# Kernel tuning notes

Hardware: AMD Instinct MI355X
Metric: run time of the kernel (lower is better)

The kernel has to match this reference:

```python
import jax, jax.numpy as jnp
import numpy as np

PROJ = 8192     # projDim
THRESH = 1e-8   # numerical-stability epsilon for signed sqrt
L2_EPS = 1e-12  # eps of torch F.normalize


def setup_inputs() -> dict:
    key = jax.random.key(0)
    k1, k2, k3, k4, k5 = jax.random.split(key, 5)
    B, C, H, W = 16, 512, 14, 14
    x = jax.random.normal(k1, (B, C, H, W), dtype=jnp.float32)
    h1 = jax.random.randint(k2, (C,), 0, PROJ, dtype=jnp.int32)
    h2 = jax.random.randint(k3, (C,), 0, PROJ, dtype=jnp.int32)
    s1 = (2 * jax.random.randint(k4, (C,), 0, 2) - 1).astype(jnp.float32)
    s2 = (2 * jax.random.randint(k5, (C,), 0, 2) - 1).astype(jnp.float32)
    return {"x": x, "s1": s1, "s2": s2, "h1": h1, "h2": h2}


def reference(x, s1, s2, h1, h2):
    # x: [B, C, H, W]; h*: [C] hash buckets in [0, PROJ); s*: [C] signs (+-1)
    B, C, H, W = x.shape
    x_flat = jnp.transpose(x, (0, 2, 3, 1)).reshape(-1, C)  # [N, C], N = B*H*W

    def count_sketch(s, h):
        # Equivalent to x_flat @ M with M[c, h[c]] = s[c]: scatter-add of
        # sign-weighted channels into PROJ bins.  -> [N, PROJ]
        return jax.ops.segment_sum((x_flat * s).T, h, num_segments=PROJ).T

    fft1 = jnp.fft.fft(count_sketch(s1, h1), axis=-1)
    fft2 = jnp.fft.fft(count_sketch(s2, h2), axis=-1)
    conv = jnp.fft.ifft(fft1 * fft2, axis=-1).real       # [N, PROJ]
    y = conv.reshape(B, H, W, PROJ).sum(axis=(1, 2))      # sum pool -> [B, PROJ]
    y = jnp.sign(y) * jnp.sqrt(jnp.abs(y) + THRESH)       # signed sqrt
    norm = jnp.linalg.norm(y, axis=1, keepdims=True)
    return y / jnp.maximum(norm, L2_EPS)                  # l2 normalize (dim=1)
```

## Files before the change

kernel.cpp:

```cpp
#include <hip/hip_runtime.h>
#include <math.h>

#define PROJ 8192
#define NB   16
#define NC   512
#define HW   196
#define KP   224
#define NROW (NB * NC)
#define XELE ((size_t)NROW * KP)

typedef __attribute__((ext_vector_type(8))) short bf16x8;
typedef __attribute__((ext_vector_type(4))) short short4v;
typedef __attribute__((ext_vector_type(4))) float f32x4;

__device__ __forceinline__ unsigned bf16_rne(float f) {
    unsigned u = __builtin_bit_cast(unsigned, f);
    return (u + 0x7fffu + ((u >> 16) & 1u)) >> 16;
}

__global__ __launch_bounds__(256)
void cbp_prep(const float* __restrict__ x,
              short* __restrict__ xh, short* __restrict__ xl) {
    const int id  = blockIdx.x * 256 + threadIdx.x;
    const int q   = id % 56;
    const int row = id / 56;
    float4 v = {0.f, 0.f, 0.f, 0.f};
    if (q < 49) v = *(const float4*)&x[(size_t)row * HW + 4 * q];
    const float f[4] = {v.x, v.y, v.z, v.w};
    short4v h, l;
#pragma unroll
    for (int c = 0; c < 4; ++c) {
        const unsigned hb = bf16_rne(f[c]);
        h[c] = (short)hb;
        l[c] = (short)bf16_rne(f[c] - __builtin_bit_cast(float, hb << 16));
    }
    *(short4v*)&xh[(size_t)row * KP + 4 * q] = h;
    *(short4v*)&xl[(size_t)row * KP + 4 * q] = l;
}

#define LOADFRAGS(buf, kc)                                             \
    {                                                                  \
        _Pragma("unroll")                                              \
        for (int i = 0; i < 2; ++i) {                                  \
            ah[buf][i] = *(const bf16x8*)&pAh[i * 3584 + (kc) * 32];   \
            al[buf][i] = *(const bf16x8*)&pAl[i * 3584 + (kc) * 32];   \
            bh[buf][i] = *(const bf16x8*)&pBh[i * 3584 + (kc) * 32];   \
            bl[buf][i] = *(const bf16x8*)&pBl[i * 3584 + (kc) * 32];   \
        }                                                              \
    }

__global__ __launch_bounds__(256, 4)
void cbp_gram(const short* __restrict__ xh, const short* __restrict__ xl,
              const float* __restrict__ s1, const float* __restrict__ s2,
              const int*   __restrict__ h1, const int*   __restrict__ h2,
              float* __restrict__ partials) {
    __shared__ float sk[PROJ];
    __shared__ int   rh1[64], rh2[64], ch1[64], ch2[64];
    __shared__ float rs1[64], rs2[64], cs1[64], cs2[64];

    const int tid = threadIdx.x;
    const int blk = blockIdx.x;
    const int xcd = blk & 7;
    const int idx = blk >> 3;
    const int hi  = (idx >= 36) ? 1 : 0;
    const int b   = 2 * xcd + hi;
    int I = 0, uu = idx - 36 * hi;
    while (uu >= 8 - I) { uu -= 8 - I; ++I; }
    const int J = I + uu;
    const int c1base = I * 64, c2base = J * 64;

    for (int i = tid; i < PROJ; i += 256) sk[i] = 0.f;
    if (tid < 64) {
        rh1[tid] = h1[c1base + tid]; rh2[tid] = h2[c1base + tid];
        rs1[tid] = s1[c1base + tid]; rs2[tid] = s2[c1base + tid];
    } else if (tid < 128) {
        const int t = tid - 64;
        ch1[t] = h1[c2base + t]; ch2[t] = h2[c2base + t];
        cs1[t] = s1[c2base + t]; cs2[t] = s2[c2base + t];
    }
    __syncthreads();

    const int lane = tid & 63, wave = tid >> 6;
    const int quad = lane >> 4, l15 = lane & 15;
    const int wr = (wave >> 1) * 32, wc = (wave & 1) * 32;

    const size_t rowA = ((size_t)b * NC + c1base + wr + l15) * KP + quad * 8;
    const size_t rowB = ((size_t)b * NC + c2base + wc + l15) * KP + quad * 8;
    const short* pAh = xh + rowA;  const short* pAl = xl + rowA;
    const short* pBh = xh + rowB;  const short* pBl = xl + rowB;

    f32x4 acc[2][2];
#pragma unroll
    for (int i = 0; i < 2; ++i)
#pragma unroll
        for (int j = 0; j < 2; ++j) acc[i][j] = (f32x4){0.f, 0.f, 0.f, 0.f};

    bf16x8 ah[2][2], al[2][2], bh[2][2], bl[2][2];
    LOADFRAGS(0, 0)
#pragma unroll
    for (int kc = 0; kc < 7; ++kc) {
        const int cur = kc & 1;
        if (kc < 6) LOADFRAGS(cur ^ 1, kc + 1)
#pragma unroll
        for (int i = 0; i < 2; ++i)
#pragma unroll
            for (int j = 0; j < 2; ++j) {
                acc[i][j] = __builtin_amdgcn_mfma_f32_16x16x32_bf16(ah[cur][i], bh[cur][j], acc[i][j], 0, 0, 0);
                acc[i][j] = __builtin_amdgcn_mfma_f32_16x16x32_bf16(ah[cur][i], bl[cur][j], acc[i][j], 0, 0, 0);
                acc[i][j] = __builtin_amdgcn_mfma_f32_16x16x32_bf16(al[cur][i], bh[cur][j], acc[i][j], 0, 0, 0);
            }
    }

    const bool offd = (I != J);
#pragma unroll
    for (int i = 0; i < 2; ++i) {
        const int r0 = wr + i * 16 + quad * 4;
#pragma unroll
        for (int j = 0; j < 2; ++j) {
            const int c = wc + j * 16 + l15;
            const int ch2v = ch2[c], ch1v = ch1[c];
            const float cs2v = cs2[c], cs1v = cs1[c];
#pragma unroll
            for (int rg = 0; rg < 4; ++rg) {
                const int r = r0 + rg;
                const float g = acc[i][j][rg];
                atomicAdd(&sk[(rh1[r] + ch2v) & (PROJ - 1)], rs1[r] * cs2v * g);
                if (offd)
                    atomicAdd(&sk[(ch1v + rh2[r]) & (PROJ - 1)], cs1v * rs2[r] * g);
            }
        }
    }
    __syncthreads();

    float4* dst = (float4*)(partials + (size_t)blk * PROJ);
    const float4* src = (const float4*)sk;
    for (int i = tid; i < PROJ / 4; i += 256) dst[i] = src[i];
}

__global__ __launch_bounds__(256)
void cbp_reduce(const float* __restrict__ partials, float* __restrict__ y,
                float* __restrict__ ssqp) {
    const int blk = blockIdx.x;
    const int xcd = blk & 7;
    const int k   = blk >> 3;
    const int hi  = k >> 5;
    const int seg = k & 31;
    const int b   = 2 * xcd + hi;
    const int tid = threadIdx.x;
    const int bin = seg * 256 + tid;

    float s = 0.f;
#pragma unroll
    for (int u = 0; u < 36; ++u) {
        int u2 = u + seg; if (u2 >= 36) u2 -= 36;
        const int pb = ((hi * 36 + u2) << 3) | xcd;
        s += partials[(size_t)pb * PROJ + bin];
    }

    const float m = sqrtf(fabsf(s) + 1e-8f);
    const float o = (s > 0.f) ? m : (s < 0.f ? -m : 0.f);
    y[b * PROJ + bin] = o;

    __shared__ float red[256];
    red[tid] = o * o;
    __syncthreads();
#pragma unroll
    for (int st = 128; st >= 1; st >>= 1) {
        if (tid < st) red[tid] += red[tid + st];
        __syncthreads();
    }
    if (tid == 0) ssqp[blk] = red[0];
}

__global__ __launch_bounds__(256)
void cbp_normalize(float* __restrict__ y, const float* __restrict__ ssqp) {
    const int b   = blockIdx.x >> 1;
    const int off = (blockIdx.x & 1) * 4096;
    const int tid = threadIdx.x;
    float ssq = 0.f;
#pragma unroll
    for (int seg = 0; seg < 32; ++seg)
        ssq += ssqp[(((b & 1) * 32 + seg) << 3) | (b >> 1)];
    const float inv = 1.0f / fmaxf(sqrtf(ssq), 1e-12f);

    float4* row = (float4*)&y[(size_t)b * PROJ + off];
#pragma unroll
    for (int j = 0; j < 4; ++j) {
        float4 v = row[j * 256 + tid];
        v.x *= inv; v.y *= inv; v.z *= inv; v.w *= inv;
        row[j * 256 + tid] = v;
    }
}

extern "C" void kernel_launch(void* const* d_in, const int* in_sizes, int n_in,
                              void* d_out, int out_size, void* d_ws, size_t ws_size,
                              hipStream_t stream) {
    const float* x  = (const float*)d_in[0];
    const float* s1 = (const float*)d_in[1];
    const float* s2 = (const float*)d_in[2];
    const int*   h1 = (const int*)d_in[3];
    const int*   h2 = (const int*)d_in[4];
    float* y = (float*)d_out;

    short* xh = (short*)d_ws;
    short* xl = xh + XELE;
    float* partials = (float*)(xl + XELE);
    float* ssqp = partials + (size_t)576 * PROJ;

    hipLaunchKernelGGL(cbp_prep, dim3(1792), dim3(256), 0, stream, x, xh, xl);
    hipLaunchKernelGGL(cbp_gram, dim3(576), dim3(256), 0, stream,
                       xh, xl, s1, s2, h1, h2, partials);
    hipLaunchKernelGGL(cbp_reduce, dim3(512), dim3(256), 0, stream,
                       partials, y, ssqp);
    hipLaunchKernelGGL(cbp_normalize, dim3(32), dim3(256), 0, stream, y, ssqp);
}
```

Before: 120.1 us.

## Compute full Gram tiles per block with 1024 threads, cutting partial sketches

```diff
diff --git a/kernel.cpp b/kernel.cpp
--- a/kernel.cpp
+++ b/kernel.cpp
@@ -6,8 +6,7 @@
 #define NC   512
 #define HW   196
 #define KP   224
-#define NROW (NB * NC)
-#define XELE ((size_t)NROW * KP)
+#define XELE ((size_t)NB * NC * KP)
 
 typedef __attribute__((ext_vector_type(8))) short bf16x8;
 typedef __attribute__((ext_vector_type(4))) short short4v;
@@ -38,54 +37,48 @@
     *(short4v*)&xl[(size_t)row * KP + 4 * q] = l;
 }
 
-#define LOADFRAGS(buf, kc)                                             \
-    {                                                                  \
-        _Pragma("unroll")                                              \
-        for (int i = 0; i < 2; ++i) {                                  \
-            ah[buf][i] = *(const bf16x8*)&pAh[i * 3584 + (kc) * 32];   \
-            al[buf][i] = *(const bf16x8*)&pAl[i * 3584 + (kc) * 32];   \
-            bh[buf][i] = *(const bf16x8*)&pBh[i * 3584 + (kc) * 32];   \
-            bl[buf][i] = *(const bf16x8*)&pBl[i * 3584 + (kc) * 32];   \
-        }                                                              \
-    }
-
-__global__ __launch_bounds__(256, 4)
+#define LOADFRAGS(buf, kc)                                          \
+    {                                                               \
+        const int off_ = (kc) * 32;                                 \
+        ah[buf][0] = *(const bf16x8*)&pAh[off_];                    \
+        ah[buf][1] = *(const bf16x8*)&pAh[16 * KP + off_];          \
+        al[buf][0] = *(const bf16x8*)&pAl[off_];                    \
+        al[buf][1] = *(const bf16x8*)&pAl[16 * KP + off_];          \
+        bh[buf][0] = *(const bf16x8*)&pBh[off_];                    \
+        bh[buf][1] = *(const bf16x8*)&pBh[16 * KP + off_];          \
+        bl[buf][0] = *(const bf16x8*)&pBl[off_];                    \
+        bl[buf][1] = *(const bf16x8*)&pBl[16 * KP + off_];          \
+    }
+
+__global__ __launch_bounds__(1024)
 void cbp_gram(const short* __restrict__ xh, const short* __restrict__ xl,
               const float* __restrict__ s1, const float* __restrict__ s2,
               const int*   __restrict__ h1, const int*   __restrict__ h2,
               float* __restrict__ partials) {
     __shared__ float sk[PROJ];
-    __shared__ int   rh1[64], rh2[64], ch1[64], ch2[64];
-    __shared__ float rs1[64], rs2[64], cs1[64], cs2[64];
 
     const int tid = threadIdx.x;
     const int blk = blockIdx.x;
     const int xcd = blk & 7;
-    const int idx = blk >> 3;
-    const int hi  = (idx >= 36) ? 1 : 0;
+    const int sub = blk >> 3;
+    const int hi  = sub >> 4;
+    const int q   = sub & 15;
     const int b   = 2 * xcd + hi;
-    int I = 0, uu = idx - 36 * hi;
-    while (uu >= 8 - I) { uu -= 8 - I; ++I; }
-    const int J = I + uu;
-    const int c1base = I * 64, c2base = J * 64;
-
-    for (int i = tid; i < PROJ; i += 256) sk[i] = 0.f;
-    if (tid < 64) {
-        rh1[tid] = h1[c1base + tid]; rh2[tid] = h2[c1base + tid];
-        rs1[tid] = s1[c1base + tid]; rs2[tid] = s2[c1base + tid];
-    } else if (tid < 128) {
-        const int t = tid - 64;
-        ch1[t] = h1[c2base + t]; ch2[t] = h2[c2base + t];
-        cs1[t] = s1[c2base + t]; cs2[t] = s2[c2base + t];
-    }
+
+    for (int i = tid; i < PROJ; i += 1024) sk[i] = 0.f;
     __syncthreads();
 
-    const int lane = tid & 63, wave = tid >> 6;
+    const int wave = tid >> 6, lane = tid & 63;
     const int quad = lane >> 4, l15 = lane & 15;
-    const int wr = (wave >> 1) * 32, wc = (wave & 1) * 32;
-
-    const size_t rowA = ((size_t)b * NC + c1base + wr + l15) * KP + quad * 8;
-    const size_t rowB = ((size_t)b * NC + c2base + wc + l15) * KP + quad * 8;
+    const int tile = q * 4 + (wave >> 2);
+    const int I = tile >> 3, J = tile & 7;
+    const int qr = ((wave >> 1) & 1) * 32;
+    const int qc = (wave & 1) * 32;
+    const int c1 = I * 64 + qr;
+    const int c2 = J * 64 + qc;
+
+    const size_t rowA = ((size_t)b * NC + c1 + l15) * KP + quad * 8;
+    const size_t rowB = ((size_t)b * NC + c2 + l15) * KP + quad * 8;
     const short* pAh = xh + rowA;  const short* pAl = xl + rowA;
     const short* pBh = xh + rowB;  const short* pBl = xl + rowB;
 
@@ -111,30 +104,37 @@
             }
     }
 
-    const bool offd = (I != J);
+    int   ha[2][4], hb[2];
+    float sa[2][4], sb[2];
 #pragma unroll
     for (int i = 0; i < 2; ++i) {
-        const int r0 = wr + i * 16 + quad * 4;
-#pragma unroll
-        for (int j = 0; j < 2; ++j) {
-            const int c = wc + j * 16 + l15;
-            const int ch2v = ch2[c], ch1v = ch1[c];
-            const float cs2v = cs2[c], cs1v = cs1[c];
+        const int r0 = c1 + i * 16 + quad * 4;
+#pragma unroll
+        for (int rg = 0; rg < 4; ++rg) {
+            ha[i][rg] = h1[r0 + rg];
+            sa[i][rg] = s1[r0 + rg];
+        }
+    }
+#pragma unroll
+    for (int j = 0; j < 2; ++j) {
+        const int c = c2 + j * 16 + l15;
+        hb[j] = h2[c];
+        sb[j] = s2[c];
+    }
+#pragma unroll
+    for (int i = 0; i < 2; ++i)
+#pragma unroll
+        for (int j = 0; j < 2; ++j)
 #pragma unroll
             for (int rg = 0; rg < 4; ++rg) {
-                const int r = r0 + rg;
-                const float g = acc[i][j][rg];
-                atomicAdd(&sk[(rh1[r] + ch2v) & (PROJ - 1)], rs1[r] * cs2v * g);
-                if (offd)
-                    atomicAdd(&sk[(ch1v + rh2[r]) & (PROJ - 1)], cs1v * rs2[r] * g);
+                const int bin = (ha[i][rg] + hb[j]) & (PROJ - 1);
+                atomicAdd(&sk[bin], sa[i][rg] * sb[j] * acc[i][j][rg]);
             }
-        }
-    }
     __syncthreads();
 
     float4* dst = (float4*)(partials + (size_t)blk * PROJ);
     const float4* src = (const float4*)sk;
-    for (int i = tid; i < PROJ / 4; i += 256) dst[i] = src[i];
+    for (int i = tid; i < PROJ / 4; i += 1024) dst[i] = src[i];
 }
 
 __global__ __launch_bounds__(256)
@@ -151,9 +151,9 @@
 
     float s = 0.f;
 #pragma unroll
-    for (int u = 0; u < 36; ++u) {
-        int u2 = u + seg; if (u2 >= 36) u2 -= 36;
-        const int pb = ((hi * 36 + u2) << 3) | xcd;
+    for (int u = 0; u < 16; ++u) {
+        const int u2 = (u + seg) & 15;
+        const int pb = ((hi * 16 + u2) << 3) | xcd;
         s += partials[(size_t)pb * PROJ + bin];
     }
 
@@ -205,10 +205,10 @@
     short* xh = (short*)d_ws;
     short* xl = xh + XELE;
     float* partials = (float*)(xl + XELE);
-    float* ssqp = partials + (size_t)576 * PROJ;
+    float* ssqp = partials + (size_t)256 * PROJ;
 
     hipLaunchKernelGGL(cbp_prep, dim3(1792), dim3(256), 0, stream, x, xh, xl);
-    hipLaunchKernelGGL(cbp_gram, dim3(576), dim3(256), 0, stream,
+    hipLaunchKernelGGL(cbp_gram, dim3(256), dim3(1024), 0, stream,
                        xh, xl, s1, s2, h1, h2, partials);
     hipLaunchKernelGGL(cbp_reduce, dim3(512), dim3(256), 0, stream,
                        partials, y, ssqp);
```

New measurement: 108.2 us. -9.9%, faster.

## Stage Gram operand tiles through LDS with coalesced loads and two-phase K split

Applied to the files above, without the earlier changes.

```diff
diff --git a/kernel.cpp b/kernel.cpp
--- a/kernel.cpp
+++ b/kernel.cpp
@@ -6,8 +6,8 @@
 #define NC   512
 #define HW   196
 #define KP   224
-#define NROW (NB * NC)
-#define XELE ((size_t)NROW * KP)
+#define LSK  132
+#define XELE ((size_t)NB * NC * KP)
 
 typedef __attribute__((ext_vector_type(8))) short bf16x8;
 typedef __attribute__((ext_vector_type(4))) short short4v;
@@ -21,9 +21,12 @@
 __global__ __launch_bounds__(256)
 void cbp_prep(const float* __restrict__ x,
               short* __restrict__ xh, short* __restrict__ xl) {
-    const int id  = blockIdx.x * 256 + threadIdx.x;
-    const int q   = id % 56;
-    const int row = id / 56;
+    const int e    = blockIdx.x & 7;
+    const int t    = blockIdx.x >> 3;
+    const int task = t * 256 + threadIdx.x;
+    const int q    = task % 56;
+    const int rp   = task / 56;
+    const int row  = e * 1024 + rp;
     float4 v = {0.f, 0.f, 0.f, 0.f};
     if (q < 49) v = *(const float4*)&x[(size_t)row * HW + 4 * q];
     const float f[4] = {v.x, v.y, v.z, v.w};
@@ -38,23 +41,14 @@
     *(short4v*)&xl[(size_t)row * KP + 4 * q] = l;
 }
 
-#define LOADFRAGS(buf, kc)                                             \
-    {                                                                  \
-        _Pragma("unroll")                                              \
-        for (int i = 0; i < 2; ++i) {                                  \
-            ah[buf][i] = *(const bf16x8*)&pAh[i * 3584 + (kc) * 32];   \
-            al[buf][i] = *(const bf16x8*)&pAl[i * 3584 + (kc) * 32];   \
-            bh[buf][i] = *(const bf16x8*)&pBh[i * 3584 + (kc) * 32];   \
-            bl[buf][i] = *(const bf16x8*)&pBl[i * 3584 + (kc) * 32];   \
-        }                                                              \
-    }
-
-__global__ __launch_bounds__(256, 4)
+__global__ __launch_bounds__(256)
 void cbp_gram(const short* __restrict__ xh, const short* __restrict__ xl,
               const float* __restrict__ s1, const float* __restrict__ s2,
               const int*   __restrict__ h1, const int*   __restrict__ h2,
               float* __restrict__ partials) {
     __shared__ float sk[PROJ];
+    __shared__ short Ah[64 * LSK], Al[64 * LSK];
+    __shared__ short Bh[64 * LSK], Bl[64 * LSK];
     __shared__ int   rh1[64], rh2[64], ch1[64], ch2[64];
     __shared__ float rs1[64], rs2[64], cs1[64], cs2[64];
 
@@ -69,7 +63,8 @@
     const int J = I + uu;
     const int c1base = I * 64, c2base = J * 64;
 
-    for (int i = tid; i < PROJ; i += 256) sk[i] = 0.f;
+    for (int i = tid; i < PROJ / 4; i += 256)
+        ((float4*)sk)[i] = (float4){0.f, 0.f, 0.f, 0.f};
     if (tid < 64) {
         rh1[tid] = h1[c1base + tid]; rh2[tid] = h2[c1base + tid];
         rs1[tid] = s1[c1base + tid]; rs2[tid] = s2[c1base + tid];
@@ -78,36 +73,95 @@
         ch1[t] = h1[c2base + t]; ch2[t] = h2[c2base + t];
         cs1[t] = s1[c2base + t]; cs2[t] = s2[c2base + t];
     }
-    __syncthreads();
+
+    const int srow = tid >> 2;
+    const int sq   = tid & 3;
+    const size_t gA = ((size_t)b * NC + c1base + srow) * KP;
+    const size_t gB = ((size_t)b * NC + c2base + srow) * KP;
+#pragma unroll
+    for (int i = 0; i < 4; ++i) {
+        const int s = sq + 4 * i;
+        *(bf16x8*)&Ah[srow * LSK + 8 * s] = *(const bf16x8*)&xh[gA + 8 * s];
+        *(bf16x8*)&Al[srow * LSK + 8 * s] = *(const bf16x8*)&xl[gA + 8 * s];
+        *(bf16x8*)&Bh[srow * LSK + 8 * s] = *(const bf16x8*)&xh[gB + 8 * s];
+        *(bf16x8*)&Bl[srow * LSK + 8 * s] = *(const bf16x8*)&xl[gB + 8 * s];
+    }
+    __syncthreads();
+
+    bf16x8 p[12];
+#pragma unroll
+    for (int i = 0; i < 3; ++i) {
+        const int s = sq + 4 * i;
+        p[4 * i + 0] = *(const bf16x8*)&xh[gA + 128 + 8 * s];
+        p[4 * i + 1] = *(const bf16x8*)&xl[gA + 128 + 8 * s];
+        p[4 * i + 2] = *(const bf16x8*)&xh[gB + 128 + 8 * s];
+        p[4 * i + 3] = *(const bf16x8*)&xl[gB + 128 + 8 * s];
+    }
 
     const int lane = tid & 63, wave = tid >> 6;
     const int quad = lane >> 4, l15 = lane & 15;
     const int wr = (wave >> 1) * 32, wc = (wave & 1) * 32;
 
-    const size_t rowA = ((size_t)b * NC + c1base + wr + l15) * KP + quad * 8;
-    const size_t rowB = ((size_t)b * NC + c2base + wc + l15) * KP + quad * 8;
-    const short* pAh = xh + rowA;  const short* pAl = xl + rowA;
-    const short* pBh = xh + rowB;  const short* pBl = xl + rowB;
-
     f32x4 acc[2][2];
 #pragma unroll
     for (int i = 0; i < 2; ++i)
 #pragma unroll
         for (int j = 0; j < 2; ++j) acc[i][j] = (f32x4){0.f, 0.f, 0.f, 0.f};
 
-    bf16x8 ah[2][2], al[2][2], bh[2][2], bl[2][2];
-    LOADFRAGS(0, 0)
-#pragma unroll
-    for (int kc = 0; kc < 7; ++kc) {
-        const int cur = kc & 1;
-        if (kc < 6) LOADFRAGS(cur ^ 1, kc + 1)
+#pragma unroll
+    for (int c = 0; c < 4; ++c) {
+        const int col = 32 * c + quad * 8;
+        bf16x8 ahf[2], alf[2], bhf[2], blf[2];
+#pragma unroll
+        for (int i = 0; i < 2; ++i) {
+            const int ra = wr + 16 * i + l15;
+            const int rb = wc + 16 * i + l15;
+            ahf[i] = *(const bf16x8*)&Ah[ra * LSK + col];
+            alf[i] = *(const bf16x8*)&Al[ra * LSK + col];
+            bhf[i] = *(const bf16x8*)&Bh[rb * LSK + col];
+            blf[i] = *(const bf16x8*)&Bl[rb * LSK + col];
+        }
 #pragma unroll
         for (int i = 0; i < 2; ++i)
 #pragma unroll
             for (int j = 0; j < 2; ++j) {
-                acc[i][j] = __builtin_amdgcn_mfma_f32_16x16x32_bf16(ah[cur][i], bh[cur][j], acc[i][j], 0, 0, 0);
-                acc[i][j] = __builtin_amdgcn_mfma_f32_16x16x32_bf16(ah[cur][i], bl[cur][j], acc[i][j], 0, 0, 0);
-                acc[i][j] = __builtin_amdgcn_mfma_f32_16x16x32_bf16(al[cur][i], bh[cur][j], acc[i][j], 0, 0, 0);
+                acc[i][j] = __builtin_amdgcn_mfma_f32_16x16x32_bf16(ahf[i], bhf[j], acc[i][j], 0, 0, 0);
+                acc[i][j] = __builtin_amdgcn_mfma_f32_16x16x32_bf16(ahf[i], blf[j], acc[i][j], 0, 0, 0);
+                acc[i][j] = __builtin_amdgcn_mfma_f32_16x16x32_bf16(alf[i], bhf[j], acc[i][j], 0, 0, 0);
+            }
+    }
+    __syncthreads();
+
+#pragma unroll
+    for (int i = 0; i < 3; ++i) {
+        const int s = sq + 4 * i;
+        *(bf16x8*)&Ah[srow * LSK + 8 * s] = p[4 * i + 0];
+        *(bf16x8*)&Al[srow * LSK + 8 * s] = p[4 * i + 1];
+        *(bf16x8*)&Bh[srow * LSK + 8 * s] = p[4 * i + 2];
+        *(bf16x8*)&Bl[srow * LSK + 8 * s] = p[4 * i + 3];
+    }
+    __syncthreads();
+
+#pragma unroll
+    for (int c = 0; c < 3; ++c) {
+        const int col = 32 * c + quad * 8;
+        bf16x8 ahf[2], alf[2], bhf[2], blf[2];
+#pragma unroll
+        for (int i = 0; i < 2; ++i) {
+            const int ra = wr + 16 * i + l15;
+            const int rb = wc + 16 * i + l15;
+            ahf[i] = *(const bf16x8*)&Ah[ra * LSK + col];
+            alf[i] = *(const bf16x8*)&Al[ra * LSK + col];
+            bhf[i] = *(const bf16x8*)&Bh[rb * LSK + col];
+            blf[i] = *(const bf16x8*)&Bl[rb * LSK + col];
+        }
+#pragma unroll
+        for (int i = 0; i < 2; ++i)
+#pragma unroll
+            for (int j = 0; j < 2; ++j) {
+                acc[i][j] = __builtin_amdgcn_mfma_f32_16x16x32_bf16(ahf[i], bhf[j], acc[i][j], 0, 0, 0);
+                acc[i][j] = __builtin_amdgcn_mfma_f32_16x16x32_bf16(ahf[i], blf[j], acc[i][j], 0, 0, 0);
+                acc[i][j] = __builtin_amdgcn_mfma_f32_16x16x32_bf16(alf[i], bhf[j], acc[i][j], 0, 0, 0);
             }
     }
 
```

New measurement: 116.1 us. 3.3% less time.
